# Kernel optimization log

Measured on AMD Instinct MI355X. Metric: run time of the kernel, lower is better.

The kernel has to match this reference:

```python
import jax, jax.numpy as jnp
import numpy as np

S, V, H = 32, 16, 8            # hidden_scalars, hidden_vectors, num_heads
N, E = 10000, 100000           # nodes, edges
NRB, RH = 16, 64               # radial basis, radial MLP hidden
TH = S + 3 * V                 # packed irreps width (80)
WNUM = S * S + V * S + S * V + 2 * V * V  # TP weight_numel = 2560


def setup_inputs() -> dict:
    key = jax.random.key(0)
    ks = jax.random.split(key, 16)
    inp = {}
    inp["node_features"] = jax.random.normal(ks[0], (N, TH), jnp.float32)
    inp["edge_index"] = jax.random.randint(ks[1], (2, E), 0, N)
    inp["edge_sh"] = jax.random.normal(ks[2], (E, 4), jnp.float32)
    inp["edge_radial"] = jax.random.uniform(ks[3], (E, NRB), dtype=jnp.float32)
    inp["edge_envelope"] = jax.random.uniform(ks[4], (E,), dtype=jnp.float32)
    # radial MLP
    inp["W1"] = jax.random.normal(ks[5], (NRB, RH), jnp.float32) / np.sqrt(NRB)
    inp["b1"] = jnp.zeros((RH,), jnp.float32)
    inp["W2"] = jax.random.normal(ks[6], (RH, WNUM), jnp.float32) / np.sqrt(RH)
    inp["b2"] = jnp.zeros((WNUM,), jnp.float32)
    # attention query/key nets (scalar channels only)
    inp["Wq"] = jax.random.normal(ks[7], (S, H), jnp.float32) / np.sqrt(S)
    inp["bq"] = jnp.zeros((H,), jnp.float32)
    inp["Wk"] = jax.random.normal(ks[8], (S, H), jnp.float32) / np.sqrt(S)
    inp["bk"] = jnp.zeros((H,), jnp.float32)
    # equivariant linears (per-irrep channel mixing, e3nn style, no bias)
    inp["Wout_s"] = jax.random.normal(ks[9], (S, S), jnp.float32)
    inp["Wout_v"] = jax.random.normal(ks[10], (V, V), jnp.float32)
    inp["Wg_s"] = jax.random.normal(ks[11], (S, S + V), jnp.float32)
    inp["Wg_v"] = jax.random.normal(ks[12], (V, V), jnp.float32)
    # equivariant batch norm params
    inp["bn_ws"] = jnp.ones((S,), jnp.float32)
    inp["bn_bs"] = jnp.zeros((S,), jnp.float32)
    inp["bn_wv"] = jnp.ones((V,), jnp.float32)
    return inp


def _forward(node_features, edge_sh, edge_radial, edge_envelope,
             W1, b1, W2, b2, Wq, bq, Wk, bk,
             Wout_s, Wout_v, Wg_s, Wg_v, bn_ws, bn_bs, bn_wv, src, dst):
    # --- per-edge TP weights from radial MLP -> (E, WNUM), the big tensor ---
    tp_w = jax.nn.silu(edge_radial @ W1 + b1) @ W2 + b2
    offs = np.cumsum([0, S * S, V * S, S * V, V * V, V * V])
    WA = tp_w[:, offs[0]:offs[1]].reshape(-1, S, S)  # 0e x 0e -> 0e
    WB = tp_w[:, offs[1]:offs[2]].reshape(-1, V, S)  # 1o x 1o -> 0e
    WC = tp_w[:, offs[2]:offs[3]].reshape(-1, S, V)  # 0e x 1o -> 1o
    WD = tp_w[:, offs[3]:offs[4]].reshape(-1, V, V)  # 1o x 0e -> 1o
    WE = tp_w[:, offs[4]:offs[5]].reshape(-1, V, V)  # 1o x 1o -> 1o (cross)

    # --- gather source features, split irreps ---
    s_src = node_features[src, :S]                       # (E, S)
    v_src = node_features[src, S:].reshape(-1, V, 3)     # (E, V, 3)
    y0 = edge_sh[:, 0:1]                                 # (E, 1) l=0
    y1 = edge_sh[:, 1:4]                                 # (E, 3) l=1

    a0 = 1.0 / np.sqrt(S + V)       # path normalization, 0e output
    a1 = 1.0 / np.sqrt(S + 2 * V)   # path normalization, 1o output

    dot = (v_src * y1[:, None, :]).sum(-1) / np.sqrt(3.0)          # (E, V)
    msg_s = a0 * (jnp.einsum('es,esk->ek', s_src * y0, WA)
                  + jnp.einsum('ev,evk->ek', dot, WB))             # (E, S)
    crs = jnp.cross(v_src, y1[:, None, :]) / np.sqrt(2.0)          # (E, V, 3)
    msg_v = a1 * (jnp.einsum('es,ec,esk->ekc', s_src, y1, WC)
                  + jnp.einsum('evc,evk->ekc', v_src * y0[:, :, None], WD)
                  + jnp.einsum('evc,evk->ekc', crs, WE))           # (E, V, 3)
    messages = jnp.concatenate([msg_s, msg_v.reshape(-1, 3 * V)], axis=-1)

    # --- scatter-softmax attention over incoming edges per destination ---
    q = node_features[dst, :S] @ Wq + bq                 # (E, H)
    k = msg_s @ Wk + bk                                  # (E, H)
    logits = (q * k).sum(-1) / np.sqrt(H) + jnp.log(edge_envelope + 1e-8)
    mx = jax.ops.segment_max(logits, dst, num_segments=N)
    ex = jnp.exp(logits - mx[dst])
    den = jax.ops.segment_sum(ex, dst, num_segments=N)
    attn = ex / (den[dst] + 1e-8)                        # (E,)

    agg = jax.ops.segment_sum(attn[:, None] * messages, dst, num_segments=N)

    # --- equivariant output linear ---
    agg_s = agg[:, :S] @ Wout_s / np.sqrt(S)
    agg_v = jnp.einsum('nvc,vw->nwc', agg[:, S:].reshape(-1, V, 3), Wout_v) / np.sqrt(V)

    # --- gate ---
    gs = agg_s @ Wg_s / np.sqrt(S)                       # (N, S+V)
    gv = jnp.einsum('nvc,vw->nwc', agg_v, Wg_v) / np.sqrt(V)
    s = jax.nn.silu(gs[:, :S])
    g = jax.nn.sigmoid(gs[:, S:])
    v = g[:, :, None] * gv
    act = jnp.concatenate([s, v.reshape(-1, 3 * V)], axis=-1)

    # --- residual + equivariant batch norm ---
    x = act + node_features
    xs = x[:, :S]
    xv = x[:, S:].reshape(-1, V, 3)
    mean = xs.mean(0)
    var = xs.var(0)
    xs = (xs - mean) / jnp.sqrt(var + 1e-5) * bn_ws + bn_bs
    vn = (xv * xv).mean(-1).mean(0)                      # (V,) component norm
    xv = xv * (bn_wv / jnp.sqrt(vn + 1e-5))[None, :, None]
    return jnp.concatenate([xs, xv.reshape(-1, 3 * V)], axis=-1)


def reference(node_features, edge_index, edge_sh, edge_radial, edge_envelope,
              W1, b1, W2, b2, Wq, bq, Wk, bk,
              Wout_s, Wout_v, Wg_s, Wg_v, bn_ws, bn_bs, bn_wv):
    src, dst = edge_index[0], edge_index[1]
    return _forward(node_features, edge_sh, edge_radial, edge_envelope,
                    W1, b1, W2, b2, Wq, bq, Wk, bk,
                    Wout_s, Wout_v, Wg_s, Wg_v, bn_ws, bn_bs, bn_wv, src, dst)
```

## Files before the change

### kernel.cpp

```cpp
#include <hip/hip_runtime.h>
#include <math.h>

typedef __bf16 bf16x8 __attribute__((ext_vector_type(8)));
typedef __bf16 bf16x4 __attribute__((ext_vector_type(4)));
typedef float  f32x4  __attribute__((ext_vector_type(4)));
typedef float  f32x2  __attribute__((ext_vector_type(2)));
typedef unsigned long long u64x2 __attribute__((ext_vector_type(2)));

__device__ __forceinline__ float silu_f(float x){ return x / (1.f + __expf(-x)); }
__device__ __forceinline__ float sigm_f(float x){ return 1.f / (1.f + __expf(-x)); }

__device__ __forceinline__ float ntld_f(const float* p){
  return __builtin_nontemporal_load(p);
}
__device__ __forceinline__ float ntbf(const __bf16* p){
  unsigned short us = __builtin_nontemporal_load((const unsigned short*)p);
  union { unsigned u; float f; } cv; cv.u = ((unsigned)us) << 16;
  return cv.f;
}
__device__ __forceinline__ void nt_store_f(float* p, float v){
  __builtin_nontemporal_store(v, p);
}
__device__ __forceinline__ void nt_store_b8(__bf16* p, bf16x8 v){
  u64x2 u; __builtin_memcpy(&u, &v, 16);
  __builtin_nontemporal_store(u, (u64x2*)p);
}
__device__ __forceinline__ f32x2 b4lo(bf16x4 v){ f32x2 r; r[0]=(float)v[0]; r[1]=(float)v[1]; return r; }
__device__ __forceinline__ f32x2 b4hi(bf16x4 v){ f32x2 r; r[0]=(float)v[2]; r[1]=(float)v[3]; return r; }

__global__ void __launch_bounds__(256) k_setup(const float* __restrict__ W2,
    __bf16* __restrict__ W2t, const int* __restrict__ ei, int* __restrict__ cnt,
    const float* __restrict__ nf, const float* __restrict__ Wq,
    const float* __restrict__ bq, const float* __restrict__ Wk,
    const float* __restrict__ bk, float* __restrict__ kvt, float* __restrict__ carr,
    int nbPrep, int nbHist, int N, int E){
  int b = blockIdx.x, t = threadIdx.x;
  if (b < nbPrep){
    __shared__ float tile[32][65];
    const int hb = b / 40, cb = b - hb*40;
    const int h0 = hb*32, col0 = cb*64;
    for (int idx = t; idx < 2048; idx += 256){
      int h = idx >> 6, col = idx & 63;
      tile[h][col] = ntld_f(&W2[(size_t)(h0+h)*2560 + col0 + col]);
    }
    __syncthreads();
    {
      int col = t >> 2, part = t & 3;
      bf16x8 o;
      #pragma unroll
      for (int j = 0; j < 8; ++j) o[j] = (__bf16)tile[part*8 + j][col];
      *(bf16x8*)(W2t + (size_t)hb*81920 + (size_t)(col0+col)*32 + part*8) = o;
    }
    return;
  }
  if (b < nbPrep + nbHist){
    int e = (b - nbPrep)*256 + t;
    if (e < E) atomicAdd(&cnt[ei[E+e]], 1);
    return;
  }
  __shared__ float M[32][33];
  __shared__ float mb[32];
  __shared__ float nfl[64][33];
  __shared__ float bqbk_s;
  const int n0 = (b - nbPrep - nbHist)*64;
  for (int idx = t; idx < 1024; idx += 256){
    int s = idx >> 5, i = idx & 31;
    float acc = 0.f;
    #pragma unroll
    for (int j = 0; j < 8; ++j) acc += Wq[s*8+j]*Wk[i*8+j];
    M[s][i] = acc;
  }
  if (t < 32){
    float acc = 0.f;
    #pragma unroll
    for (int j = 0; j < 8; ++j) acc += Wq[t*8+j]*bk[j];
    mb[t] = acc;
  }
  if (t == 0){
    float acc = 0.f;
    #pragma unroll
    for (int j = 0; j < 8; ++j) acc += bq[j]*bk[j];
    bqbk_s = acc;
  }
  for (int idx = t; idx < 2048; idx += 256){
    int nl = idx >> 5, s = idx & 31;
    int n = n0 + nl;
    nfl[nl][s] = (n < N) ? nf[(size_t)n*80 + s] : 0.f;
  }
  __syncthreads();
  for (int idx = t; idx < 2048; idx += 256){
    int nl = idx >> 5, i = idx & 31;
    int n = n0 + nl;
    if (n < N){
      float acc = 0.f;
      #pragma unroll 8
      for (int s = 0; s < 32; ++s) acc += nfl[nl][s]*M[s][i];
      kvt[(size_t)n*32 + i] = acc;
    }
  }
  if (t < 64){
    int n = n0 + t;
    if (n < N){
      float acc = bqbk_s;
      #pragma unroll 8
      for (int s = 0; s < 32; ++s) acc += nfl[t][s]*mb[s];
      carr[n] = acc;
    }
  }
}

__global__ void __launch_bounds__(1024) k_scan(const int* __restrict__ cnt,
    int* __restrict__ cursor, float* __restrict__ bnacc, int N, int E){
  __shared__ int part[1024];
  int t = threadIdx.x;
  if (t < 80) bnacc[t] = 0.f;
  int chunk = (N + 1023) >> 10;
  int lo = t*chunk, hi = min(lo+chunk, N);
  int s = 0;
  for (int i = lo; i < hi; ++i) s += cnt[i];
  part[t] = s;
  __syncthreads();
  for (int off = 1; off < 1024; off <<= 1){
    int v = (t >= off) ? part[t-off] : 0;
    __syncthreads();
    part[t] += v;
    __syncthreads();
  }
  int base = (t == 0) ? 0 : part[t-1];
  for (int i = lo; i < hi; ++i){
    cursor[i] = base;
    base += cnt[i];
  }
}

__global__ void __launch_bounds__(256, 4) k_prep(
    const float* __restrict__ nf, const int* __restrict__ ei,
    const float* __restrict__ sh, const float* __restrict__ radial,
    const float* __restrict__ W1, const float* __restrict__ b1,
    int* __restrict__ cursor,
    __bf16* __restrict__ uG, __bf16* __restrict__ cabG, __bf16* __restrict__ cvG,
    int* __restrict__ permG, int E, int NT)
{
  __shared__ float featT[80][65];
  __shared__ float radl[64][17];
  __shared__ float shlT[4][64];
  __shared__ float w1l[1024];
  __shared__ float b1l[64];
  __shared__ __align__(16) __bf16 u_l[64][72];
  __shared__ int src_l[64];

  const int t = threadIdx.x;
  const int e0 = blockIdx.x*64;
  const int tg0 = blockIdx.x*4;

  if (t < 64){
    int ee = e0 + t;
    if (ee < E){
      src_l[t] = ei[ee];
      permG[ee] = atomicAdd(&cursor[ei[(size_t)E+ee]], 1);
    } else src_l[t] = ei[E-1];
    b1l[t] = b1[t];
  }
  {
    int e = t >> 2, c = t & 3;
    int ec = min(e0+e, E-1);
    shlT[c][e] = ntld_f(&sh[(size_t)ec*4+c]);
  }
  for (int i = t; i < 1024; i += 256){
    int e = i >> 4, r = i & 15;
    int ec = min(e0+e, E-1);
    radl[e][r] = ntld_f(&radial[(size_t)ec*16+r]);
  }
  *(float4*)&w1l[t*4] = ((const float4*)W1)[t];
  __syncthreads();

  for (int i = t; i < 1280; i += 256){
    int e = i / 20, q = i - e*20;
    float4 v = *(const float4*)&nf[(size_t)src_l[e]*80 + q*4];
    featT[q*4+0][e] = v.x;
    featT[q*4+1][e] = v.y;
    featT[q*4+2][e] = v.z;
    featT[q*4+3][e] = v.w;
  }
  for (int i = t; i < 4096; i += 256){
    int e = i & 63, h = i >> 6;
    float acc = b1l[h];
    #pragma unroll
    for (int r = 0; r < 16; ++r) acc += radl[e][r]*w1l[r*64+h];
    u_l[e][h] = (__bf16)silu_f(acc);
  }
  __syncthreads();

  const float inv_s3 = 0.57735026918962576f;
  const float inv_s2 = 0.70710678118654752f;
  const float a0 = 0.14433756729740643f;
  const float a1 = 0.125f;

  for (int i = t; i < 512; i += 256){
    int tl = i >> 7, rem = i & 127, k8 = rem >> 4, e = rem & 15;
    if (tg0 + tl < NT){
      bf16x8 v = *(const bf16x8*)&u_l[tl*16 + e][k8*8];
      *(bf16x8*)((char*)uG + (size_t)(tg0+tl)*2048 + k8*256 + e*16) = v;
    }
  }
  for (int i = t; i < 384; i += 256){
    int h = i & 1, tl = (i >> 1) & 3, r = i >> 3;
    if (tg0 + tl >= NT) continue;
    bf16x8 o;
    #pragma unroll
    for (int j = 0; j < 8; ++j){
      int e = tl*16 + h*8 + j;
      float val;
      if (r < 32) val = a0 * shlT[0][e] * featT[r][e];
      else {
        int v = r - 32;
        float dot = (featT[32+v*3][e]*shlT[1][e] + featT[33+v*3][e]*shlT[2][e]
                   + featT[34+v*3][e]*shlT[3][e]) * inv_s3;
        val = a0 * dot;
      }
      o[j] = (__bf16)val;
    }
    *(bf16x8*)((char*)cabG + (size_t)(tg0+tl)*1536 + r*32 + h*16) = o;
  }
  for (int i = t; i < 1536; i += 256){
    int h = i & 1, tl = (i >> 1) & 3, c = (i >> 3) % 3, r = i / 24;
    if (tg0 + tl >= NT) continue;
    int c1 = c+1; if (c1 > 2) c1 -= 3;
    int c2 = c+2; if (c2 > 2) c2 -= 3;
    bf16x8 o;
    #pragma unroll
    for (int j = 0; j < 8; ++j){
      int e = tl*16 + h*8 + j;
      float val;
      if (r < 32) val = a1 * shlT[1+c][e] * featT[r][e];
      else if (r < 48){
        int v = r - 32;
        val = a1 * shlT[0][e] * featT[32+v*3+c][e];
      } else {
        int v = r - 48;
        val = a1 * inv_s2 * (featT[32+v*3+c1][e]*shlT[1+c2][e]
                           - featT[32+v*3+c2][e]*shlT[1+c1][e]);
      }
      o[j] = (__bf16)val;
    }
    *(bf16x8*)((char*)cvG + (size_t)(tg0+tl)*6144 + r*96 + c*32 + h*16) = o;
  }
}

#define LOAD_PANEL(BASE_IT, NITS) do {                                         \
    for (int idx = t; idx < (NITS)*128; idx += 1024){                          \
      int itl_ = idx >> 7, rem_ = idx & 127, half_ = rem_ >> 6, r6_ = rem_ & 63;\
      int col_ = r6_ >> 2, quad_ = r6_ & 3;                                    \
      *(float4*)(panel + itl_*2048 + half_*1024 + quad_*256 + col_*16) =       \
        *(const float4*)(w2b + half_*163840 + (size_t)((BASE_IT)+itl_)*1024    \
                         + col_*64 + quad_*16);                                \
    }                                                                          \
    for (int i = t; i < (NITS)*16; i += 1024) b2l[i] = b2[(BASE_IT)*16 + i];   \
  } while(0)

#define CAB_STAGE(TGC, BASE) do {                                              \
    bf16x8 x_ = *(const bf16x8*)(cabGb + (size_t)(TGC)*1536 + lane*16);        \
    bf16x4 y_ = *(const bf16x4*)(cabGb + (size_t)(TGC)*1536 + 1024 + lane*8);  \
    *(bf16x8*)(myCab + (BASE) + lane*16) = x_;                                 \
    *(bf16x4*)(myCab + (BASE) + 1024 + lane*8) = y_;                           \
  } while(0)

#define CV_STAGE_SUB(TGC, BASE, HALF, SUB) do {                                \
    const char* s_ = cvGb + (size_t)(TGC)*6144 + (HALF)*3072 + (SUB)*1536      \
                   + lane*24;                                                  \
    bf16x4 a_ = *(const bf16x4*)(s_);                                          \
    bf16x4 b_ = *(const bf16x4*)(s_ + 8);                                      \
    bf16x4 c_ = *(const bf16x4*)(s_ + 16);                                     \
    *(bf16x4*)(myCab + (BASE) + lane*24)      = a_;                            \
    *(bf16x4*)(myCab + (BASE) + lane*24 + 8)  = b_;                            \
    *(bf16x4*)(myCab + (BASE) + lane*24 + 16) = c_;                            \
  } while(0)

#define S_PAIR(SECOND, CBA, CBB, TA, TB) do {                                  \
    _Pragma("unroll 4")                                                        \
    for (int itl = 0; itl < 48; ++itl){                                        \
      bf16x8 B0_ = *(const bf16x8*)(panel + itl*2048 + laneOff);               \
      bf16x8 B1_ = *(const bf16x8*)(panel + itl*2048 + 1024 + laneOff);        \
      f32x4 dA_; dA_[0]=0;dA_[1]=0;dA_[2]=0;dA_[3]=0; f32x4 dB_ = dA_;         \
      dA_ = __builtin_amdgcn_mfma_f32_16x16x32_bf16(u##TA##_0, B0_, dA_, 0,0,0);\
      dB_ = __builtin_amdgcn_mfma_f32_16x16x32_bf16(u##TB##_0, B0_, dB_, 0,0,0);\
      dA_ = __builtin_amdgcn_mfma_f32_16x16x32_bf16(u##TA##_1, B1_, dA_, 0,0,0);\
      dB_ = __builtin_amdgcn_mfma_f32_16x16x32_bf16(u##TB##_1, B1_, dB_, 0,0,0);\
      const float bias_ = b2l[itl*16 + nlo];                                   \
      f32x2 bb_; bb_[0]=bias_; bb_[1]=bias_;                                   \
      f32x2 dAlo_ = __builtin_shufflevector(dA_,dA_,0,1) + bb_;                \
      f32x2 dAhi_ = __builtin_shufflevector(dA_,dA_,2,3) + bb_;                \
      f32x2 dBlo_ = __builtin_shufflevector(dB_,dB_,0,1) + bb_;                \
      f32x2 dBhi_ = __builtin_shufflevector(dB_,dB_,2,3) + bb_;                \
      const int r_ = (SECOND)*24 + (itl>>1);                                   \
      bf16x4 cA_ = *(const bf16x4*)(myCab + (CBA) + r_*32 + quad*8);           \
      bf16x4 cB_ = *(const bf16x4*)(myCab + (CBB) + r_*32 + quad*8);           \
      if (itl & 1){                                                            \
        s1l##TA += b4lo(cA_)*dAlo_; s1h##TA += b4hi(cA_)*dAhi_;                \
        s1l##TB += b4lo(cB_)*dBlo_; s1h##TB += b4hi(cB_)*dBhi_;                \
      } else {                                                                 \
        s0l##TA += b4lo(cA_)*dAlo_; s0h##TA += b4hi(cA_)*dAhi_;                \
        s0l##TB += b4lo(cB_)*dBlo_; s0h##TB += b4hi(cB_)*dBhi_;                \
      }                                                                        \
    }                                                                          \
  } while(0)

#define V_PAIR_SUB(SUB, TA, TB) do {                                           \
    _Pragma("unroll 4")                                                        \
    for (int il = 0; il < 16; ++il){                                           \
      const int gitl = (SUB)*16 + il;                                          \
      bf16x8 B0_ = *(const bf16x8*)(panel + gitl*2048 + laneOff);              \
      bf16x8 B1_ = *(const bf16x8*)(panel + gitl*2048 + 1024 + laneOff);       \
      f32x4 dA_; dA_[0]=0;dA_[1]=0;dA_[2]=0;dA_[3]=0; f32x4 dB_ = dA_;         \
      dA_ = __builtin_amdgcn_mfma_f32_16x16x32_bf16(u##TA##_0, B0_, dA_, 0,0,0);\
      dB_ = __builtin_amdgcn_mfma_f32_16x16x32_bf16(u##TB##_0, B0_, dB_, 0,0,0);\
      dA_ = __builtin_amdgcn_mfma_f32_16x16x32_bf16(u##TA##_1, B1_, dA_, 0,0,0);\
      dB_ = __builtin_amdgcn_mfma_f32_16x16x32_bf16(u##TB##_1, B1_, dB_, 0,0,0);\
      const float bias_ = b2l[gitl*16 + nlo];                                  \
      f32x2 bb_; bb_[0]=bias_; bb_[1]=bias_;                                   \
      f32x2 dAlo_ = __builtin_shufflevector(dA_,dA_,0,1) + bb_;                \
      f32x2 dAhi_ = __builtin_shufflevector(dA_,dA_,2,3) + bb_;                \
      f32x2 dBlo_ = __builtin_shufflevector(dB_,dB_,0,1) + bb_;                \
      f32x2 dBhi_ = __builtin_shufflevector(dB_,dB_,2,3) + bb_;                \
      const char* cbA_ = myCab + il*96;                                        \
      const char* cbB_ = myCab + 1536 + il*96;                                 \
      bf16x4 q0_ = *(const bf16x4*)(cbA_ + quad*8);                            \
      bf16x4 q1_ = *(const bf16x4*)(cbA_ + 32 + quad*8);                       \
      bf16x4 q2_ = *(const bf16x4*)(cbA_ + 64 + quad*8);                       \
      v0l##TA += b4lo(q0_)*dAlo_; v0h##TA += b4hi(q0_)*dAhi_;                  \
      v1l##TA += b4lo(q1_)*dAlo_; v1h##TA += b4hi(q1_)*dAhi_;                  \
      v2l##TA += b4lo(q2_)*dAlo_; v2h##TA += b4hi(q2_)*dAhi_;                  \
      q0_ = *(const bf16x4*)(cbB_ + quad*8);                                   \
      q1_ = *(const bf16x4*)(cbB_ + 32 + quad*8);                              \
      q2_ = *(const bf16x4*)(cbB_ + 64 + quad*8);                              \
      v0l##TB += b4lo(q0_)*dBlo_; v0h##TB += b4hi(q0_)*dBhi_;                  \
      v1l##TB += b4lo(q1_)*dBlo_; v1h##TB += b4hi(q1_)*dBhi_;                  \
      v2l##TB += b4lo(q2_)*dBlo_; v2h##TB += b4hi(q2_)*dBhi_;                  \
    }                                                                          \
  } while(0)

#define S_FLUSH(TG, S0LO, S0HI, S1LO, S1HI) do {                               \
      myOut[(eb+0)*56 + nlo] = S0LO[0];                                        \
      myOut[(eb+1)*56 + nlo] = S0LO[1];                                        \
      myOut[(eb+2)*56 + nlo] = S0HI[0];                                        \
      myOut[(eb+3)*56 + nlo] = S0HI[1];                                        \
      myOut[(eb+0)*56 + 16+nlo] = S1LO[0];                                     \
      myOut[(eb+1)*56 + 16+nlo] = S1LO[1];                                     \
      myOut[(eb+2)*56 + 16+nlo] = S1HI[0];                                     \
      myOut[(eb+3)*56 + 16+nlo] = S1HI[1];                                     \
      const int e0e = (TG)*16;                                                 \
      { int e = lane>>2, seg = lane&3, eg = e0e + e;                           \
        if (eg < E){                                                           \
          f32x4 m0 = *(const f32x4*)&myOut[e*56 + seg*8];                      \
          f32x4 m1 = *(const f32x4*)&myOut[e*56 + seg*8 + 4];                  \
          bf16x8 o; o[0]=(__bf16)m0[0]; o[1]=(__bf16)m0[1];                    \
          o[2]=(__bf16)m0[2]; o[3]=(__bf16)m0[3]; o[4]=(__bf16)m1[0];          \
          o[5]=(__bf16)m1[1]; o[6]=(__bf16)m1[2]; o[7]=(__bf16)m1[3];          \
          nt_store_b8(msgs + (size_t)permG[eg]*80 + seg*8, o);                 \
        } }                                                                    \
      for (int r8 = 0; r8 < 2; ++r8){                                          \
        int e = r8*8 + (lane>>3), kq = lane&7, eg = e0e + e;                   \
        f32x4 ms = *(const f32x4*)&myOut[e*56 + kq*4];                         \
        int dn = ei[(size_t)E + min(eg, E-1)];                                 \
        const float* kvp = kvt + (size_t)dn*32 + kq*4;                         \
        float part = ms[0]*kvp[0]+ms[1]*kvp[1]+ms[2]*kvp[2]+ms[3]*kvp[3];      \
        part += __shfl_xor(part, 1);                                           \
        part += __shfl_xor(part, 2);                                           \
        part += __shfl_xor(part, 4);                                           \
        if (kq == 0 && eg < E){                                                \
          float lg = (part + carr[dn]) * 0.35355339059327373f                  \
                   + logf(ntld_f(&env[eg]) + 1e-8f);                           \
          nt_store_f(&logits_s[permG[eg]], lg);                                \
        } }                                                                    \
  } while(0)

#define V_FLUSH(TG, V0LO, V0HI, V1LO, V1HI, V2LO, V2HI) do {                   \
      const int cb2 = nlo*3;                                                   \
      myOut[(eb+0)*56 + cb2+0] = V0LO[0];                                      \
      myOut[(eb+1)*56 + cb2+0] = V0LO[1];                                      \
      myOut[(eb+2)*56 + cb2+0] = V0HI[0];                                      \
      myOut[(eb+3)*56 + cb2+0] = V0HI[1];                                      \
      myOut[(eb+0)*56 + cb2+1] = V1LO[0];                                      \
      myOut[(eb+1)*56 + cb2+1] = V1LO[1];                                      \
      myOut[(eb+2)*56 + cb2+1] = V1HI[0];                                      \
      myOut[(eb+3)*56 + cb2+1] = V1HI[1];                                      \
      myOut[(eb+0)*56 + cb2+2] = V2LO[0];                                      \
      myOut[(eb+1)*56 + cb2+2] = V2LO[1];                                      \
      myOut[(eb+2)*56 + cb2+2] = V2HI[0];                                      \
      myOut[(eb+3)*56 + cb2+2] = V2HI[1];                                      \
      const int e0e = (TG)*16;                                                 \
      for (int i = lane; i < 96; i += 64){                                     \
        int e = i/6, seg = i - (i/6)*6, eg = e0e + e;                          \
        if (eg < E){                                                           \
          f32x4 m0 = *(const f32x4*)&myOut[e*56 + seg*8];                      \
          f32x4 m1 = *(const f32x4*)&myOut[e*56 + seg*8 + 4];                  \
          bf16x8 o; o[0]=(__bf16)m0[0]; o[1]=(__bf16)m0[1];                    \
          o[2]=(__bf16)m0[2]; o[3]=(__bf16)m0[3]; o[4]=(__bf16)m1[0];          \
          o[5]=(__bf16)m1[1]; o[6]=(__bf16)m1[2]; o[7]=(__bf16)m1[3];          \
          nt_store_b8(msgs + (size_t)permG[eg]*80 + 32 + seg*8, o);            \
        } }                                                                    \
  } while(0)

__global__ void __launch_bounds__(1024, 4) k_edge(
    const __bf16* __restrict__ W2t, const float* __restrict__ b2,
    const __bf16* __restrict__ uG, const __bf16* __restrict__ cabG,
    const __bf16* __restrict__ cvG, const int* __restrict__ ei,
    const int* __restrict__ permG, const float* __restrict__ kvt,
    const float* __restrict__ carr, const float* __restrict__ env,
    __bf16* __restrict__ msgs, float* __restrict__ logits_s, int E, int NT)
{
  __shared__ __align__(16) char panel[98304];
  __shared__ __align__(16) char wstage[16][3584];
  __shared__ float b2l[768];

  const int t = threadIdx.x;
  const int lane = t & 63;
  const int wv   = t >> 6;
  const int quad = lane >> 4;
  const int nlo  = lane & 15;
  const int wgid = blockIdx.x*16 + wv;
  const int laneOff = quad*256 + nlo*16;
  const int uOff    = quad*256 + nlo*16;
  char*  myCab = wstage[wv];
  float* myOut = (float*)wstage[wv];
  const char* w2b   = (const char*)W2t;
  const char* uGb   = (const char*)uG;
  const char* cabGb = (const char*)cabG;
  const char* cvGb  = (const char*)cvG;

  const int tA = wgid, tB = wgid + 4096;
  const bool hA = tA < NT, hB = tB < NT;
  const int cA = min(tA, NT-1), cB = min(tB, NT-1);

  const bf16x8 uA_0 = *(const bf16x8*)(uGb + (size_t)cA*2048 + uOff);
  const bf16x8 uA_1 = *(const bf16x8*)(uGb + (size_t)cA*2048 + 1024 + uOff);
  const bf16x8 uB_0 = *(const bf16x8*)(uGb + (size_t)cB*2048 + uOff);
  const bf16x8 uB_1 = *(const bf16x8*)(uGb + (size_t)cB*2048 + 1024 + uOff);

  f32x2 s0lA={0,0}, s0hA={0,0}, s1lA={0,0}, s1hA={0,0};
  f32x2 s0lB={0,0}, s0hB={0,0}, s1lB={0,0}, s1hB={0,0};

  const int eb = quad*4;

  LOAD_PANEL(0, 48);
  CAB_STAGE(cA, 0); CAB_STAGE(cB, 1536);
  __syncthreads();
  S_PAIR(0, 0, 1536, A, B);
  __syncthreads();
  LOAD_PANEL(48, 48);
  __syncthreads();
  S_PAIR(1, 0, 1536, A, B);
  if (hA) S_FLUSH(tA, s0lA, s0hA, s1lA, s1hA);
  if (hB) S_FLUSH(tB, s0lB, s0hB, s1lB, s1hB);
  __syncthreads();

  f32x2 v0lA={0,0}, v0hA={0,0}, v1lA={0,0}, v1hA={0,0}, v2lA={0,0}, v2hA={0,0};
  f32x2 v0lB={0,0}, v0hB={0,0}, v1lB={0,0}, v1hB={0,0}, v2lB={0,0}, v2hB={0,0};

  LOAD_PANEL(96, 32);
  __syncthreads();
  CV_STAGE_SUB(cA, 0, 0, 0); CV_STAGE_SUB(cB, 1536, 0, 0);
  V_PAIR_SUB(0, A, B);
  CV_STAGE_SUB(cA, 0, 0, 1); CV_STAGE_SUB(cB, 1536, 0, 1);
  V_PAIR_SUB(1, A, B);
  __syncthreads();
  LOAD_PANEL(128, 32);
  __syncthreads();
  CV_STAGE_SUB(cA, 0, 1, 0); CV_STAGE_SUB(cB, 1536, 1, 0);
  V_PAIR_SUB(0, A, B);
  CV_STAGE_SUB(cA, 0, 1, 1); CV_STAGE_SUB(cB, 1536, 1, 1);
  V_PAIR_SUB(1, A, B);
  if (hA) V_FLUSH(tA, v0lA, v0hA, v1lA, v1hA, v2lA, v2hA);
  if (hB) V_FLUSH(tB, v0lB, v0hB, v1lB, v1hB, v2lB, v2hB);
}

__global__ void __launch_bounds__(256) k_agg(
    const __bf16* __restrict__ msgs, const float* __restrict__ logits_s,
    const int* __restrict__ cursor, const float* __restrict__ nf,
    const float* __restrict__ Wout_s, const float* __restrict__ Wout_v,
    const float* __restrict__ Wg_s, const float* __restrict__ Wg_v,
    float* __restrict__ xbuf, float* __restrict__ bnacc, int N)
{
  __shared__ float aggl[4][80];
  __shared__ float t1[4][96];
  __shared__ float t2[4][96];
  __shared__ float bnl[80];
  const int t = threadIdx.x, l = t & 63, wv = t >> 6;
  const int n = blockIdx.x*4 + wv;
  const bool act = (n < N);
  const int nc = act ? n : (N-1);
  if (t < 80) bnl[t] = 0.f;

  const int r0 = (nc == 0) ? 0 : cursor[nc-1];
  const int r1 = cursor[nc];
  const int deg = act ? (r1 - r0) : 0;

  float mym = -3.4e38f;
  for (int i = l; i < deg; i += 64) mym = fmaxf(mym, logits_s[r0+i]);
  #pragma unroll
  for (int s = 32; s; s >>= 1) mym = fmaxf(mym, __shfl_xor(mym, s));
  float denp = 0.f, acc0 = 0.f, acc1 = 0.f;
  for (int c0 = 0; c0 < deg; c0 += 64){
    const int len = min(64, deg - c0);
    float ex = 0.f;
    if (l < len) ex = __expf(logits_s[r0+c0+l] - mym);
    denp += ex;
    for (int j0 = 0; j0 < len; j0 += 4){
      const int jn = len - j0;
      const __bf16* base = msgs + (size_t)(r0+c0+j0)*80;
      float v0=0,v1=0,v2=0,v3=0, w0=0,w1=0,w2=0,w3=0;
      float a0_=0,a1_=0,a2_=0,a3_=0;
      v0 = ntbf(&base[l]); if (l < 16) w0 = ntbf(&base[64+l]); a0_ = __shfl(ex, j0);
      if (jn > 1){ v1 = ntbf(&base[80+l]);  if (l < 16) w1 = ntbf(&base[144+l]); a1_ = __shfl(ex, j0+1); }
      if (jn > 2){ v2 = ntbf(&base[160+l]); if (l < 16) w2 = ntbf(&base[224+l]); a2_ = __shfl(ex, j0+2); }
      if (jn > 3){ v3 = ntbf(&base[240+l]); if (l < 16) w3 = ntbf(&base[304+l]); a3_ = __shfl(ex, j0+3); }
      acc0 += a0_*v0 + a1_*v1 + a2_*v2 + a3_*v3;
      if (l < 16) acc1 += a0_*w0 + a1_*w1 + a2_*w2 + a3_*w3;
    }
  }
  #pragma unroll
  for (int s = 32; s; s >>= 1) denp += __shfl_xor(denp, s);
  const float inv = 1.f/(denp + 1e-8f);
  aggl[wv][l] = acc0 * inv;
  if (l < 16) aggl[wv][64+l] = acc1 * inv;
  __syncthreads();

  const float* arow = &aggl[wv][0];
  const float iS = 0.17677669529663687f;
  const float iV = 0.25f;
  for (int o = l; o < 80; o += 64){
    float val = 0.f;
    if (o < 32){
      for (int s = 0; s < 32; ++s) val += arow[s]*Wout_s[s*32+o];
      val *= iS;
    } else {
      int w = (o-32)/3, c = (o-32)-w*3;
      for (int v = 0; v < 16; ++v) val += arow[32+v*3+c]*Wout_v[v*16+w];
      val *= iV;
    }
    t1[wv][o] = val;
  }
  __syncthreads();
  for (int o = l; o < 96; o += 64){
    float val = 0.f;
    if (o < 48){
      for (int k = 0; k < 32; ++k) val += t1[wv][k]*Wg_s[k*48+o];
      val *= iS;
    } else {
      int w = (o-48)/3, c = (o-48)-w*3;
      for (int v = 0; v < 16; ++v) val += t1[wv][32+v*3+c]*Wg_v[v*16+w];
      val *= iV;
    }
    t2[wv][o] = val;
  }
  __syncthreads();
  for (int o = l; o < 80; o += 64){
    float x;
    if (o < 32){
      x = silu_f(t2[wv][o]) + nf[(size_t)nc*80+o];
      if (act){
        nt_store_f(&xbuf[(size_t)n*80+o], x);
        atomicAdd(&bnl[o], x);
        atomicAdd(&bnl[32+o], x*x);
      }
    } else {
      int w = (o-32)/3;
      x = sigm_f(t2[wv][32+w]) * t2[wv][48+(o-32)] + nf[(size_t)nc*80+o];
      if (act){
        nt_store_f(&xbuf[(size_t)n*80+o], x);
        atomicAdd(&bnl[64+w], x*x);
      }
    }
  }
  __syncthreads();
  if (t < 80) atomicAdd(&bnacc[t], bnl[t]);
}

__global__ void __launch_bounds__(256) k_out(const float* __restrict__ xbuf,
    const float* __restrict__ bnacc,
    const float* __restrict__ bn_ws, const float* __restrict__ bn_bs,
    const float* __restrict__ bn_wv, float* __restrict__ out, int N){
  __shared__ float coef[80];
  int t = threadIdx.x;
  float fN = (float)N;
  if (t < 32){
    float mean = bnacc[t]/fN;
    float var = bnacc[32+t]/fN - mean*mean;
    float cm = bn_ws[t]*rsqrtf(var + 1e-5f);
    coef[t] = cm;
    coef[32+t] = bn_bs[t] - mean*cm;
  } else if (t < 48){
    int v = t - 32;
    coef[64+v] = bn_wv[v]*rsqrtf(bnacc[64+v]/(3.f*fN) + 1e-5f);
  }
  __syncthreads();
  int i = blockIdx.x*256 + t;
  if (i >= N*80) return;
  int o = i - (i/80)*80;
  float x = ntld_f(&xbuf[i]);
  nt_store_f(&out[i], (o < 32) ? (x*coef[o] + coef[32+o]) : (x*coef[64+(o-32)/3]));
}

extern "C" void kernel_launch(void* const* d_in, const int* in_sizes, int n_in,
                              void* d_out, int out_size, void* d_ws, size_t ws_size,
                              hipStream_t stream) {
  const float* nf     = (const float*)d_in[0];
  const int*   ei     = (const int*)  d_in[1];
  const float* sh     = (const float*)d_in[2];
  const float* radial = (const float*)d_in[3];
  const float* env    = (const float*)d_in[4];
  const float* W1     = (const float*)d_in[5];
  const float* b1     = (const float*)d_in[6];
  const float* W2     = (const float*)d_in[7];
  const float* b2     = (const float*)d_in[8];
  const float* Wq     = (const float*)d_in[9];
  const float* bq     = (const float*)d_in[10];
  const float* Wk     = (const float*)d_in[11];
  const float* bk     = (const float*)d_in[12];
  const float* Wout_s = (const float*)d_in[13];
  const float* Wout_v = (const float*)d_in[14];
  const float* Wg_s   = (const float*)d_in[15];
  const float* Wg_v   = (const float*)d_in[16];
  const float* bn_ws  = (const float*)d_in[17];
  const float* bn_bs  = (const float*)d_in[18];
  const float* bn_wv  = (const float*)d_in[19];

  const int E = in_sizes[4];
  const int N = in_sizes[0] / 80;
  const int NT = (E + 15)/16;

  float* ws = (float*)d_ws;
  size_t off = 0;
  __bf16* w2t    = (__bf16*)(ws + off); off += 81920;
  __bf16* msgs   = (__bf16*)(ws + off); off += (size_t)E*40;
  float* logits_s= ws + off; off += E;
  int* cnt       = (int*)(ws + off); off += N;
  int* cursor    = (int*)(ws + off); off += N;
  float* xbuf    = ws + off; off += (size_t)N*80;
  float* bnacc   = ws + off; off += 80;
  float* kvt     = ws + off; off += (size_t)N*32;
  float* carr    = ws + off; off += N;
  int* permG     = (int*)(ws + off); off += E;
  __bf16* uG     = (__bf16*)(ws + off); off += (size_t)NT*512;
  __bf16* cabG   = (__bf16*)(ws + off); off += (size_t)NT*384;
  __bf16* cvG    = (__bf16*)(ws + off); off += (size_t)NT*1536;

  hipMemsetAsync(cnt, 0, (size_t)N*sizeof(int), stream);

  const int nbPrep = 80;
  const int nbHist = (E + 255)/256;
  const int nbKv   = (N + 63)/64;
  k_setup<<<nbPrep + nbHist + nbKv, 256, 0, stream>>>(W2, w2t, ei, cnt,
      nf, Wq, bq, Wk, bk, kvt, carr, nbPrep, nbHist, N, E);
  k_scan<<<1, 1024, 0, stream>>>(cnt, cursor, bnacc, N, E);
  k_prep<<<(E + 63)/64, 256, 0, stream>>>(nf, ei, sh, radial, W1, b1, cursor,
      uG, cabG, cvG, permG, E, NT);
  k_edge<<<256, 1024, 0, stream>>>(w2t, b2, uG, cabG, cvG, ei, permG,
      kvt, carr, env, msgs, logits_s, E, NT);
  k_agg<<<(N + 3)/4, 256, 0, stream>>>(msgs, logits_s, cursor, nf,
      Wout_s, Wout_v, Wg_s, Wg_v, xbuf, bnacc, N);
  k_out<<<(N*80 + 255)/256, 256, 0, stream>>>(xbuf, bnacc, bn_ws, bn_bs, bn_wv,
      (float*)d_out, N);
}
```

Before: 317.8 us.

## Interleave paired edge tiles in coefficient buffers for wide loads

k_prep now writes the cab and cv coefficient buffers in a paired-tile layout, with the A and B tiles handled by one wave interleaved at 4-element granularity. k_edge stages each pair with 16-byte loads and reads both tiles' coefficients with a single bf16x8 LDS load that is then split. Tile assignment changes from (wgid, wgid+4096) to adjacent tiles (2*wgid, 2*wgid+1), which keeps the two tiles contiguous in memory. The goal is fewer, wider global and LDS transactions, paid for by more complex scattered stores in k_prep.

Result: no change. 318.6 us (+0.2%).

```diff
diff --git a/kernel.cpp b/kernel.cpp
--- a/kernel.cpp
+++ b/kernel.cpp
@@ -138,7 +138,7 @@
     const float* __restrict__ sh, const float* __restrict__ radial,
     const float* __restrict__ W1, const float* __restrict__ b1,
     int* __restrict__ cursor,
-    __bf16* __restrict__ uG, __bf16* __restrict__ cabG, __bf16* __restrict__ cvG,
+    __bf16* __restrict__ uG, __bf16* __restrict__ cabP, __bf16* __restrict__ cvP,
     int* __restrict__ permG, int E, int NT)
 {
   __shared__ float featT[80][65];
@@ -220,7 +220,11 @@
       }
       o[j] = (__bf16)val;
     }
-    *(bf16x8*)((char*)cabG + (size_t)(tg0+tl)*1536 + r*32 + h*16) = o;
+    bf16x4 lo = __builtin_shufflevector(o, o, 0,1,2,3);
+    bf16x4 hi = __builtin_shufflevector(o, o, 4,5,6,7);
+    char* base = (char*)cabP + (size_t)((tg0>>1) + (tl>>1))*3072 + r*64 + (tl&1)*8;
+    *(bf16x4*)(base + (2*h)*16)   = lo;
+    *(bf16x4*)(base + (2*h+1)*16) = hi;
   }
   for (int i = t; i < 1536; i += 256){
     int h = i & 1, tl = (i >> 1) & 3, c = (i >> 3) % 3, r = i / 24;
@@ -243,7 +247,15 @@
       }
       o[j] = (__bf16)val;
     }
-    *(bf16x8*)((char*)cvG + (size_t)(tg0+tl)*6144 + r*96 + c*32 + h*16) = o;
+    bf16x4 lo = __builtin_shufflevector(o, o, 0,1,2,3);
+    bf16x4 hi = __builtin_shufflevector(o, o, 4,5,6,7);
+    char* rbase = (char*)cvP + (size_t)((tg0>>1) + (tl>>1))*12288 + r*192;
+    int ab = tl & 1;
+    char *w0, *w1;
+    if (c < 2){ w0 = rbase + ab*64 + (2*h)*16 + c*8;  w1 = rbase + ab*64 + (2*h+1)*16 + c*8; }
+    else      { w0 = rbase + 128   + (2*h)*16 + ab*8; w1 = rbase + 128   + (2*h+1)*16 + ab*8; }
+    *(bf16x4*)w0 = lo;
+    *(bf16x4*)w1 = hi;
   }
 }
 
@@ -258,25 +270,28 @@
     for (int i = t; i < (NITS)*16; i += 1024) b2l[i] = b2[(BASE_IT)*16 + i];   \
   } while(0)
 
-#define CAB_STAGE(TGC, BASE) do {                                              \
-    bf16x8 x_ = *(const bf16x8*)(cabGb + (size_t)(TGC)*1536 + lane*16);        \
-    bf16x4 y_ = *(const bf16x4*)(cabGb + (size_t)(TGC)*1536 + 1024 + lane*8);  \
-    *(bf16x8*)(myCab + (BASE) + lane*16) = x_;                                 \
-    *(bf16x4*)(myCab + (BASE) + 1024 + lane*8) = y_;                           \
+#define CAB_STAGEP() do {                                                      \
+    const char* s_ = cabPb + (size_t)pc*3072 + lane*48;                        \
+    bf16x8 a_ = *(const bf16x8*)(s_);                                          \
+    bf16x8 b_ = *(const bf16x8*)(s_ + 16);                                     \
+    bf16x8 c_ = *(const bf16x8*)(s_ + 32);                                     \
+    *(bf16x8*)(myCab + lane*48)      = a_;                                     \
+    *(bf16x8*)(myCab + lane*48 + 16) = b_;                                     \
+    *(bf16x8*)(myCab + lane*48 + 32) = c_;                                     \
   } while(0)
 
-#define CV_STAGE_SUB(TGC, BASE, HALF, SUB) do {                                \
-    const char* s_ = cvGb + (size_t)(TGC)*6144 + (HALF)*3072 + (SUB)*1536      \
-                   + lane*24;                                                  \
-    bf16x4 a_ = *(const bf16x4*)(s_);                                          \
-    bf16x4 b_ = *(const bf16x4*)(s_ + 8);                                      \
-    bf16x4 c_ = *(const bf16x4*)(s_ + 16);                                     \
-    *(bf16x4*)(myCab + (BASE) + lane*24)      = a_;                            \
-    *(bf16x4*)(myCab + (BASE) + lane*24 + 8)  = b_;                            \
-    *(bf16x4*)(myCab + (BASE) + lane*24 + 16) = c_;                            \
+#define CV_STAGEP(SUB, HALF) do {                                              \
+    const char* s_ = cvPb + (size_t)pc*12288 + ((HALF)*32 + (SUB)*16)*192      \
+                   + lane*48;                                                  \
+    bf16x8 a_ = *(const bf16x8*)(s_);                                          \
+    bf16x8 b_ = *(const bf16x8*)(s_ + 16);                                     \
+    bf16x8 c_ = *(const bf16x8*)(s_ + 32);                                     \
+    *(bf16x8*)(myCab + lane*48)      = a_;                                     \
+    *(bf16x8*)(myCab + lane*48 + 16) = b_;                                     \
+    *(bf16x8*)(myCab + lane*48 + 32) = c_;                                     \
   } while(0)
 
-#define S_PAIR(SECOND, CBA, CBB, TA, TB) do {                                  \
+#define S_PAIR(SECOND, TA, TB) do {                                            \
     _Pragma("unroll 4")                                                        \
     for (int itl = 0; itl < 48; ++itl){                                        \
       bf16x8 B0_ = *(const bf16x8*)(panel + itl*2048 + laneOff);               \
@@ -293,8 +308,9 @@
       f32x2 dBlo_ = __builtin_shufflevector(dB_,dB_,0,1) + bb_;                \
       f32x2 dBhi_ = __builtin_shufflevector(dB_,dB_,2,3) + bb_;                \
       const int r_ = (SECOND)*24 + (itl>>1);                                   \
-      bf16x4 cA_ = *(const bf16x4*)(myCab + (CBA) + r_*32 + quad*8);           \
-      bf16x4 cB_ = *(const bf16x4*)(myCab + (CBB) + r_*32 + quad*8);           \
+      bf16x8 c8_ = *(const bf16x8*)(myCab + r_*64 + quad*16);                  \
+      bf16x4 cA_ = __builtin_shufflevector(c8_, c8_, 0,1,2,3);                 \
+      bf16x4 cB_ = __builtin_shufflevector(c8_, c8_, 4,5,6,7);                 \
       if (itl & 1){                                                            \
         s1l##TA += b4lo(cA_)*dAlo_; s1h##TA += b4hi(cA_)*dAhi_;                \
         s1l##TB += b4lo(cB_)*dBlo_; s1h##TB += b4hi(cB_)*dBhi_;                \
@@ -322,20 +338,22 @@
       f32x2 dAhi_ = __builtin_shufflevector(dA_,dA_,2,3) + bb_;                \
       f32x2 dBlo_ = __builtin_shufflevector(dB_,dB_,0,1) + bb_;                \
       f32x2 dBhi_ = __builtin_shufflevector(dB_,dB_,2,3) + bb_;                \
-      const char* cbA_ = myCab + il*96;                                        \
-      const char* cbB_ = myCab + 1536 + il*96;                                 \
-      bf16x4 q0_ = *(const bf16x4*)(cbA_ + quad*8);                            \
-      bf16x4 q1_ = *(const bf16x4*)(cbA_ + 32 + quad*8);                       \
-      bf16x4 q2_ = *(const bf16x4*)(cbA_ + 64 + quad*8);                       \
-      v0l##TA += b4lo(q0_)*dAlo_; v0h##TA += b4hi(q0_)*dAhi_;                  \
-      v1l##TA += b4lo(q1_)*dAlo_; v1h##TA += b4hi(q1_)*dAhi_;                  \
-      v2l##TA += b4lo(q2_)*dAlo_; v2h##TA += b4hi(q2_)*dAhi_;                  \
-      q0_ = *(const bf16x4*)(cbB_ + quad*8);                                   \
-      q1_ = *(const bf16x4*)(cbB_ + 32 + quad*8);                              \
-      q2_ = *(const bf16x4*)(cbB_ + 64 + quad*8);                              \
-      v0l##TB += b4lo(q0_)*dBlo_; v0h##TB += b4hi(q0_)*dBhi_;                  \
-      v1l##TB += b4lo(q1_)*dBlo_; v1h##TB += b4hi(q1_)*dBhi_;                  \
-      v2l##TB += b4lo(q2_)*dBlo_; v2h##TB += b4hi(q2_)*dBhi_;                  \
+      const char* rb_ = myCab + il*192;                                        \
+      bf16x8 a01_ = *(const bf16x8*)(rb_ + quad*16);                           \
+      bf16x8 b01_ = *(const bf16x8*)(rb_ + 64 + quad*16);                      \
+      bf16x8 c2_  = *(const bf16x8*)(rb_ + 128 + quad*16);                     \
+      bf16x4 q0A_ = __builtin_shufflevector(a01_, a01_, 0,1,2,3);              \
+      bf16x4 q1A_ = __builtin_shufflevector(a01_, a01_, 4,5,6,7);              \
+      bf16x4 q0B_ = __builtin_shufflevector(b01_, b01_, 0,1,2,3);              \
+      bf16x4 q1B_ = __builtin_shufflevector(b01_, b01_, 4,5,6,7);              \
+      bf16x4 q2A_ = __builtin_shufflevector(c2_, c2_, 0,1,2,3);                \
+      bf16x4 q2B_ = __builtin_shufflevector(c2_, c2_, 4,5,6,7);                \
+      v0l##TA += b4lo(q0A_)*dAlo_; v0h##TA += b4hi(q0A_)*dAhi_;                \
+      v1l##TA += b4lo(q1A_)*dAlo_; v1h##TA += b4hi(q1A_)*dAhi_;                \
+      v2l##TA += b4lo(q2A_)*dAlo_; v2h##TA += b4hi(q2A_)*dAhi_;                \
+      v0l##TB += b4lo(q0B_)*dBlo_; v0h##TB += b4hi(q0B_)*dBhi_;                \
+      v1l##TB += b4lo(q1B_)*dBlo_; v1h##TB += b4hi(q1B_)*dBhi_;                \
+      v2l##TB += b4lo(q2B_)*dBlo_; v2h##TB += b4hi(q2B_)*dBhi_;                \
     }                                                                          \
   } while(0)
 
@@ -403,8 +421,8 @@
 
 __global__ void __launch_bounds__(1024, 4) k_edge(
     const __bf16* __restrict__ W2t, const float* __restrict__ b2,
-    const __bf16* __restrict__ uG, const __bf16* __restrict__ cabG,
-    const __bf16* __restrict__ cvG, const int* __restrict__ ei,
+    const __bf16* __restrict__ uG, const __bf16* __restrict__ cabP,
+    const __bf16* __restrict__ cvP, const int* __restrict__ ei,
     const int* __restrict__ permG, const float* __restrict__ kvt,
     const float* __restrict__ carr, const float* __restrict__ env,
     __bf16* __restrict__ msgs, float* __restrict__ logits_s, int E, int NT)
@@ -425,10 +443,12 @@
   float* myOut = (float*)wstage[wv];
   const char* w2b   = (const char*)W2t;
   const char* uGb   = (const char*)uG;
-  const char* cabGb = (const char*)cabG;
-  const char* cvGb  = (const char*)cvG;
-
-  const int tA = wgid, tB = wgid + 4096;
+  const char* cabPb = (const char*)cabP;
+  const char* cvPb  = (const char*)cvP;
+
+  const int NP = (NT + 1) >> 1;
+  const int pc = min(wgid, NP-1);
+  const int tA = 2*wgid, tB = 2*wgid + 1;
   const bool hA = tA < NT, hB = tB < NT;
   const int cA = min(tA, NT-1), cB = min(tB, NT-1);
 
@@ -443,13 +463,13 @@
   const int eb = quad*4;
 
   LOAD_PANEL(0, 48);
-  CAB_STAGE(cA, 0); CAB_STAGE(cB, 1536);
-  __syncthreads();
-  S_PAIR(0, 0, 1536, A, B);
+  CAB_STAGEP();
+  __syncthreads();
+  S_PAIR(0, A, B);
   __syncthreads();
   LOAD_PANEL(48, 48);
   __syncthreads();
-  S_PAIR(1, 0, 1536, A, B);
+  S_PAIR(1, A, B);
   if (hA) S_FLUSH(tA, s0lA, s0hA, s1lA, s1hA);
   if (hB) S_FLUSH(tB, s0lB, s0hB, s1lB, s1hB);
   __syncthreads();
@@ -459,16 +479,16 @@
 
   LOAD_PANEL(96, 32);
   __syncthreads();
-  CV_STAGE_SUB(cA, 0, 0, 0); CV_STAGE_SUB(cB, 1536, 0, 0);
+  CV_STAGEP(0, 0);
   V_PAIR_SUB(0, A, B);
-  CV_STAGE_SUB(cA, 0, 0, 1); CV_STAGE_SUB(cB, 1536, 0, 1);
+  CV_STAGEP(1, 0);
   V_PAIR_SUB(1, A, B);
   __syncthreads();
   LOAD_PANEL(128, 32);
   __syncthreads();
-  CV_STAGE_SUB(cA, 0, 1, 0); CV_STAGE_SUB(cB, 1536, 1, 0);
+  CV_STAGEP(0, 1);
   V_PAIR_SUB(0, A, B);
-  CV_STAGE_SUB(cA, 0, 1, 1); CV_STAGE_SUB(cB, 1536, 1, 1);
+  CV_STAGEP(1, 1);
   V_PAIR_SUB(1, A, B);
   if (hA) V_FLUSH(tA, v0lA, v0hA, v1lA, v1hA, v2lA, v2hA);
   if (hB) V_FLUSH(tB, v0lB, v0hB, v1lB, v1hB, v2lB, v2hB);
@@ -628,6 +648,7 @@
   const int E = in_sizes[4];
   const int N = in_sizes[0] / 80;
   const int NT = (E + 15)/16;
+  const int NP = (NT + 1)/2;
 
   float* ws = (float*)d_ws;
   size_t off = 0;
@@ -642,8 +663,8 @@
   float* carr    = ws + off; off += N;
   int* permG     = (int*)(ws + off); off += E;
   __bf16* uG     = (__bf16*)(ws + off); off += (size_t)NT*512;
-  __bf16* cabG   = (__bf16*)(ws + off); off += (size_t)NT*384;
-  __bf16* cvG    = (__bf16*)(ws + off); off += (size_t)NT*1536;
+  __bf16* cabP   = (__bf16*)(ws + off); off += (size_t)NP*768;
+  __bf16* cvP    = (__bf16*)(ws + off); off += (size_t)NP*3072;
 
   hipMemsetAsync(cnt, 0, (size_t)N*sizeof(int), stream);
 
@@ -654,8 +675,8 @@
       nf, Wq, bq, Wk, bk, kvt, carr, nbPrep, nbHist, N, E);
   k_scan<<<1, 1024, 0, stream>>>(cnt, cursor, bnacc, N, E);
   k_prep<<<(E + 63)/64, 256, 0, stream>>>(nf, ei, sh, radial, W1, b1, cursor,
-      uG, cabG, cvG, permG, E, NT);
-  k_edge<<<256, 1024, 0, stream>>>(w2t, b2, uG, cabG, cvG, ei, permG,
+      uG, cabP, cvP, permG, E, NT);
+  k_edge<<<256, 1024, 0, stream>>>(w2t, b2, uG, cabP, cvP, ei, permG,
       kvt, carr, env, msgs, logits_s, E, NT);
   k_agg<<<(N + 3)/4, 256, 0, stream>>>(msgs, logits_s, cursor, nf,
       Wout_s, Wout_v, Wg_s, Wg_v, xbuf, bnacc, N);
```
